# Optimization experiments

Hardware: AMD Instinct MI355X
Metric: run time of the kernel (lower is better)

The kernel has to match this reference:

```python
import jax, jax.numpy as jnp
import numpy as np

DET = 512       # detector bins
N_THETA = 180   # projection angles, theta = 0..179 degrees (1 deg spacing)


def _ramp_filter(size):
    """skimage _get_fourier_filter(size, 'ramp'): spatial ramp -> FFT."""
    n = np.concatenate((np.arange(1, size // 2 + 1, 2),
                        np.arange(size // 2 - 1, 0, -2)))
    f = np.zeros(size)
    f[0] = 0.25
    f[1::2] = -1.0 / (np.pi * n) ** 2
    return jnp.asarray(2.0 * np.real(np.fft.fft(f)), dtype=jnp.float32)


def _iradon(x):
    B, C, det, A = x.shape
    theta = jnp.deg2rad(jnp.arange(A, dtype=jnp.float32))  # 0..179 deg

    # --- ramp filtering along the detector axis ---
    size = max(64, int(2 ** np.ceil(np.log2(2 * det))))  # 1024 for det=512
    filt = _ramp_filter(size)                            # (size,)
    xp = jnp.pad(x, ((0, 0), (0, 0), (0, size - det), (0, 0)))
    proj_f = jnp.fft.fft(xp, axis=2) * filt[None, None, :, None]
    filtered = jnp.real(jnp.fft.ifft(proj_f, axis=2))[:, :, :det, :]  # (B,C,det,A)

    # --- backprojection (circle=False) ---
    out_size = int(np.floor(np.sqrt(det ** 2 / 2.0)))  # 362
    radius = out_size // 2
    xpr = jnp.arange(out_size, dtype=jnp.float32)[:, None] - radius  # rows
    ypr = jnp.arange(out_size, dtype=jnp.float32)[None, :] - radius  # cols
    cos_t = jnp.cos(theta)
    sin_t = jnp.sin(theta)
    # detector coordinate for every (angle, pixel): t = y*cos - x*sin
    t = ypr[None] * cos_t[:, None, None] - xpr[None] * sin_t[:, None, None]  # (A,out,out)
    pos = t + det // 2          # index into detector axis (x = arange(det)-det//2)
    i0 = jnp.floor(pos).astype(jnp.int32)
    frac = pos - i0.astype(jnp.float32)
    in_range = ((pos >= 0) & (pos <= det - 1)).astype(jnp.float32)  # fill_value=0 outside
    i0c = jnp.clip(i0, 0, det - 1)
    i1c = jnp.clip(i0 + 1, 0, det - 1)

    P = out_size * out_size
    ft = jnp.moveaxis(filtered, 3, 2)                     # (B,C,A,det)
    idx0 = jnp.broadcast_to(i0c.reshape(A, P)[None, None], (B, C, A, P))
    idx1 = jnp.broadcast_to(i1c.reshape(A, P)[None, None], (B, C, A, P))
    g0 = jnp.take_along_axis(ft, idx0, axis=3)            # (B,C,A,P)
    g1 = jnp.take_along_axis(ft, idx1, axis=3)
    w = frac.reshape(A, P)[None, None]
    m = in_range.reshape(A, P)[None, None]
    val = ((1.0 - w) * g0 + w * g1) * m                   # bilinear-in-1D interp, 0 outside
    recon = val.sum(axis=2).reshape(B, C, out_size, out_size)
    return recon * (jnp.pi / (2.0 * A))


def setup_inputs() -> dict:
    key = jax.random.key(0)
    x = jax.random.normal(key, (4, 1, DET, N_THETA), dtype=jnp.float32)
    return {"x": x}


def reference(x):
    return _iradon(x)
```

## Files before the change

kernel.cpp:

```cpp
#include <hip/hip_runtime.h>
#include <math.h>

#define DET 512
#define NA  180
#define OUT 362
#define RAD 181

#define NSPLIT 3
#define APB    60
#define CHUNK  10
#define LSTRIDE 516

constexpr double PI_D = 3.14159265358979323846;

constexpr double tsin(double x) {
    double x2 = x * x;
    return x * (1.0 + x2 * (-1.0/6 + x2 * (1.0/120 + x2 * (-1.0/5040 +
               x2 * (1.0/362880 + x2 * (-1.0/39916800))))));
}
constexpr double tcos(double x) {
    double x2 = x * x;
    return 1.0 + x2 * (-0.5 + x2 * (1.0/24 + x2 * (-1.0/720 +
               x2 * (1.0/40320 + x2 * (-1.0/3628800)))));
}

struct alignas(16) Trig { float c[NA]; float s[NA]; };
constexpr Trig make_trig() {
    Trig t{};
    constexpr double r = PI_D / 180.0;
    for (int k = 0; k < NA; ++k) {
        double c, s;
        if (k <= 45)       { c =  tcos(k * r);          s =  tsin(k * r); }
        else if (k <= 90)  { c =  tsin((90 - k) * r);   s =  tcos((90 - k) * r); }
        else if (k <= 135) { c = -tsin((k - 90) * r);   s =  tcos((k - 90) * r); }
        else               { c = -tcos((180 - k) * r);  s =  tsin((180 - k) * r); }
        t.c[k] = (float)c; t.s[k] = (float)s;
    }
    return t;
}
__device__ constexpr Trig TRIG = make_trig();

struct alignas(16) WTab { float w[2 * 127 * 8]; };
constexpr WTab make_wtab() {
    WTab t{};
    for (int h = 0; h < 2; ++h)
        for (int ui = 0; ui < 127; ++ui)
            for (int di = 0; di < 8; ++di) {
                int m = 8 * (ui - 63) + 2 * (di - 3) - 1 + 2 * h;
                double md = (double)m;
                t.w[(h * 127 + ui) * 8 + di] =
                    (float)(-2.0 / (PI_D * PI_D * md * md));
            }
    return t;
}
__device__ constexpr WTab WTAB = make_wtab();

__global__ __launch_bounds__(128) void ramp_filter_kernel(
        const float* __restrict__ x, float* __restrict__ ft,
        float* __restrict__ out, int n4, int pb4) {
    const int bx = blockIdx.x;
    const int b  = blockIdx.y;
    const int t  = threadIdx.x;

    const int rr = bx & 7, qq = bx >> 3;
    const int a  = 22 * rr + min(rr, 4) + qq;

    {
        float4* oz = (float4*)out;
        const float4 z4 = make_float4(0.f, 0.f, 0.f, 0.f);
        const int base4 = (b * NA + bx) * pb4;
        for (int i = t; i < pb4; i += 128) {
            int idx = base4 + i;
            if (idx < n4) oz[idx] = z4;
        }
    }

    __shared__ float Ef[768];
    __shared__ float Of[768];

    const float2 z2 = make_float2(0.f, 0.f);
    *(float2*)&Ef[2 * t]       = z2;
    *(float2*)&Ef[512 + 2 * t] = z2;
    *(float2*)&Of[2 * t]       = z2;
    *(float2*)&Of[512 + 2 * t] = z2;

    const float* xc = x + (size_t)(b * DET) * NA + a;
    float v0 = xc[(4 * t + 0) * NA];
    float v1 = xc[(4 * t + 1) * NA];
    float v2 = xc[(4 * t + 2) * NA];
    float v3 = xc[(4 * t + 3) * NA];
    *(float2*)&Ef[256 + 2 * t] = make_float2(v0, v2);
    *(float2*)&Of[256 + 2 * t] = make_float2(v1, v3);
    __syncthreads();

    const int half = __builtin_amdgcn_readfirstlane(t >> 6);
    const int tp   = t & 63;
    const float4* src4  = (const float4*)(half ? Ef : Of);
    const float4* self4 = (const float4*)(half ? Of : Ef);
    const float* __restrict__ Wh = WTAB.w + half * (127 * 8);

    float acc0 = 0.f, acc1 = 0.f, acc2 = 0.f, acc3 = 0.f;
    #pragma unroll 2
    for (int ui = 0; ui < 127; ++ui) {
        const float4 w0 = *(const float4*)&Wh[ui * 8];
        const float4 w1 = *(const float4*)&Wh[ui * 8 + 4];
        float4 s4 = src4[tp + (127 - ui)];
        acc0 = fmaf(s4.x, w0.w, fmaf(s4.y, w0.z, fmaf(s4.z, w0.y, fmaf(s4.w, w0.x, acc0))));
        acc1 = fmaf(s4.x, w1.x, fmaf(s4.y, w0.w, fmaf(s4.z, w0.z, fmaf(s4.w, w0.y, acc1))));
        acc2 = fmaf(s4.x, w1.y, fmaf(s4.y, w1.x, fmaf(s4.z, w0.w, fmaf(s4.w, w0.z, acc2))));
        acc3 = fmaf(s4.x, w1.z, fmaf(s4.y, w1.y, fmaf(s4.z, w1.x, fmaf(s4.w, w0.w, acc3))));
    }

    float4 sf = self4[64 + tp];
    acc0 = fmaf(0.5f, sf.x, acc0);
    acc1 = fmaf(0.5f, sf.y, acc1);
    acc2 = fmaf(0.5f, sf.z, acc2);
    acc3 = fmaf(0.5f, sf.w, acc3);

    float* o = ft + (b * NA + a) * DET + 8 * tp + half;
    o[0] = acc0;
    o[2] = acc1;
    o[4] = acc2;
    o[6] = acc3;
}

__device__ __forceinline__ float interp_fast(const float* __restrict__ L, float pos) {
    float fr = __builtin_amdgcn_fractf(pos);
    int   i0 = (int)pos;
    float g0 = L[i0];
    float g1 = L[i0 + 1];
    return fmaf(fr, g1 - g0, g0);
}
__device__ __forceinline__ float interp_masked(const float* __restrict__ L, float pos) {
    float v = interp_fast(L, pos);
    return pos <= (float)(DET - 1) ? v : 0.0f;
}

__global__ __launch_bounds__(256) void backproject_kernel(
        const float* __restrict__ ft, float* __restrict__ out) {
    const int bz = blockIdx.z;
    const int b  = bz / NSPLIT;
    const int sp = bz - b * NSPLIT;
    const int r0 = blockIdx.y * 32;
    const int c0 = blockIdx.x * 32;
    const int tid = threadIdx.x;
    const int tx = tid & 15;
    const int ty = tid >> 4;

    __shared__ float line[CHUNK][LSTRIDE];

    if (tid < CHUNK) line[tid][512] = 0.0f;

    const float xpr = (float)(min(r0 + ty, OUT - 1) - RAD);
    const float ypr = (float)(min(c0 + tx, OUT - 1) - RAD);

    float a00 = 0.0f, a01 = 0.0f, a10 = 0.0f, a11 = 0.0f;

    const float* base = ft + (b * NA + sp * APB) * DET;

    auto run = [&](auto&& interp) {
        for (int rd = 0; rd < APB / CHUNK; ++rd) {
            __syncthreads();
            const float* gsrc = base + rd * CHUNK * DET;
            #pragma unroll
            for (int k = 0; k < 5; ++k) {
                int j4 = tid + k * 256;
                float4 v = *(const float4*)&gsrc[j4 * 4];
                int ci = j4 >> 7;
                int d  = (j4 & 127) << 2;
                *(float4*)&line[ci][d] = v;
            }
            __syncthreads();

            const int abase = sp * APB + rd * CHUNK;
            #pragma unroll
            for (int i = 0; i < CHUNK; ++i) {
                const float cv = TRIG.c[abase + i];
                const float sv = TRIG.s[abase + i];
                float p00 = fmaf(ypr, cv, fmaf(xpr, -sv, 256.0f));
                float p01 = fmaf(16.0f, cv, p00);
                float p10 = fmaf(-16.0f, sv, p00);
                float p11 = fmaf(-16.0f, sv, p01);
                const float* L = line[i];
                a00 += interp(L, p00);
                a01 += interp(L, p01);
                a10 += interp(L, p10);
                a11 += interp(L, p11);
            }
        }
    };

    {
        float drm = fmaxf(fabsf((float)(r0 - RAD)),
                          fabsf((float)(min(r0 + 31, OUT - 1) - RAD)));
        float dcm = fmaxf(fabsf((float)(c0 - RAD)),
                          fabsf((float)(min(c0 + 31, OUT - 1) - RAD)));
        if (drm * drm + dcm * dcm <= 65025.0f)
            run([](const float* __restrict__ L, float p) { return interp_fast(L, p); });
        else
            run([](const float* __restrict__ L, float p) { return interp_masked(L, p); });
    }

    const float scale = (float)(PI_D / (2.0 * NA));
    const int r = r0 + ty;
    const int c = c0 + tx;
    float* ob = out + b * OUT * OUT;
    if (r < OUT) {
        if (c < OUT)      atomicAdd(&ob[r * OUT + c],      a00 * scale);
        if (c + 16 < OUT) atomicAdd(&ob[r * OUT + c + 16], a01 * scale);
    }
    if (r + 16 < OUT) {
        if (c < OUT)      atomicAdd(&ob[(r + 16) * OUT + c],      a10 * scale);
        if (c + 16 < OUT) atomicAdd(&ob[(r + 16) * OUT + c + 16], a11 * scale);
    }
}

extern "C" void kernel_launch(void* const* d_in, const int* in_sizes, int n_in,
                              void* d_out, int out_size, void* d_ws, size_t ws_size,
                              hipStream_t stream) {
    const float* x = (const float*)d_in[0];
    float* ft  = (float*)d_ws;
    float* out = (float*)d_out;

    const int B = in_sizes[0] / (DET * NA);

    const int n4  = out_size / 4;
    const int pb4 = (n4 + NA * B - 1) / (NA * B);

    ramp_filter_kernel<<<dim3(NA, B), 128, 0, stream>>>(x, ft, out, n4, pb4);
    backproject_kernel<<<dim3((OUT + 31) / 32, (OUT + 31) / 32, B * NSPLIT),
                         256, 0, stream>>>(ft, out);
}
```

Before: 109.8 us.

## Store filtered sinogram as neighbor pairs and gather directly from global memory

The filter kernel now writes each detector sample together with its right neighbour as a float2 (padded row stride), so backprojection can fetch both interpolation taps with one 8-byte load. Backprojection drops its LDS staging and block barriers and reads the paired rows straight from global/L2 memory. The filter kernel also doubles its threads and splits the convolution loop across two waves, combining partial sums through shared memory. The trade-off is that gathers now depend on cache hit rates rather than LDS, and the workspace is twice as large.

Result: slower. 121.1 us (+10.3%).

```diff
diff --git a/kernel.cpp b/kernel.cpp
--- a/kernel.cpp
+++ b/kernel.cpp
@@ -8,8 +8,7 @@
 
 #define NSPLIT 3
 #define APB    60
-#define CHUNK  10
-#define LSTRIDE 516
+#define FTP_LD 516
 
 constexpr double PI_D = 3.14159265358979323846;
 
@@ -55,8 +54,8 @@
 }
 __device__ constexpr WTab WTAB = make_wtab();
 
-__global__ __launch_bounds__(128) void ramp_filter_kernel(
-        const float* __restrict__ x, float* __restrict__ ft,
+__global__ __launch_bounds__(256) void ramp_filter_kernel(
+        const float* __restrict__ x, float2* __restrict__ ftp,
         float* __restrict__ out, int n4, int pb4) {
     const int bx = blockIdx.x;
     const int b  = blockIdx.y;
@@ -69,7 +68,7 @@
         float4* oz = (float4*)out;
         const float4 z4 = make_float4(0.f, 0.f, 0.f, 0.f);
         const int base4 = (b * NA + bx) * pb4;
-        for (int i = t; i < pb4; i += 128) {
+        for (int i = t; i < pb4; i += 256) {
             int idx = base4 + i;
             if (idx < n4) oz[idx] = z4;
         }
@@ -77,31 +76,30 @@
 
     __shared__ float Ef[768];
     __shared__ float Of[768];
-
-    const float2 z2 = make_float2(0.f, 0.f);
-    *(float2*)&Ef[2 * t]       = z2;
-    *(float2*)&Ef[512 + 2 * t] = z2;
-    *(float2*)&Of[2 * t]       = z2;
-    *(float2*)&Of[512 + 2 * t] = z2;
+    __shared__ float4 Rbuf[2][64];
+
+    Ef[t] = 0.f;  Ef[512 + t] = 0.f;
+    Of[t] = 0.f;  Of[512 + t] = 0.f;
 
     const float* xc = x + (size_t)(b * DET) * NA + a;
-    float v0 = xc[(4 * t + 0) * NA];
-    float v1 = xc[(4 * t + 1) * NA];
-    float v2 = xc[(4 * t + 2) * NA];
-    float v3 = xc[(4 * t + 3) * NA];
-    *(float2*)&Ef[256 + 2 * t] = make_float2(v0, v2);
-    *(float2*)&Of[256 + 2 * t] = make_float2(v1, v3);
+    float ev = xc[(2 * t) * NA];
+    float ov = xc[(2 * t + 1) * NA];
+    Ef[256 + t] = ev;
+    Of[256 + t] = ov;
     __syncthreads();
 
-    const int half = __builtin_amdgcn_readfirstlane(t >> 6);
+    const int half = __builtin_amdgcn_readfirstlane(t >> 7);
+    const int wseg = __builtin_amdgcn_readfirstlane((t >> 6) & 1);
     const int tp   = t & 63;
     const float4* src4  = (const float4*)(half ? Ef : Of);
     const float4* self4 = (const float4*)(half ? Of : Ef);
     const float* __restrict__ Wh = WTAB.w + half * (127 * 8);
 
     float acc0 = 0.f, acc1 = 0.f, acc2 = 0.f, acc3 = 0.f;
+    const int uiBeg = wseg ? 64 : 0;
+    const int uiEnd = wseg ? 127 : 64;
     #pragma unroll 2
-    for (int ui = 0; ui < 127; ++ui) {
+    for (int ui = uiBeg; ui < uiEnd; ++ui) {
         const float4 w0 = *(const float4*)&Wh[ui * 8];
         const float4 w1 = *(const float4*)&Wh[ui * 8 + 4];
         float4 s4 = src4[tp + (127 - ui)];
@@ -111,33 +109,44 @@
         acc3 = fmaf(s4.x, w1.z, fmaf(s4.y, w1.y, fmaf(s4.z, w1.x, fmaf(s4.w, w0.w, acc3))));
     }
 
-    float4 sf = self4[64 + tp];
-    acc0 = fmaf(0.5f, sf.x, acc0);
-    acc1 = fmaf(0.5f, sf.y, acc1);
-    acc2 = fmaf(0.5f, sf.z, acc2);
-    acc3 = fmaf(0.5f, sf.w, acc3);
-
-    float* o = ft + (b * NA + a) * DET + 8 * tp + half;
-    o[0] = acc0;
-    o[2] = acc1;
-    o[4] = acc2;
-    o[6] = acc3;
-}
-
-__device__ __forceinline__ float interp_fast(const float* __restrict__ L, float pos) {
+    if (wseg) {
+        Rbuf[half][tp] = make_float4(acc0, acc1, acc2, acc3);
+    } else {
+        float4 sf = self4[64 + tp];
+        acc0 = fmaf(0.5f, sf.x, acc0);
+        acc1 = fmaf(0.5f, sf.y, acc1);
+        acc2 = fmaf(0.5f, sf.z, acc2);
+        acc3 = fmaf(0.5f, sf.w, acc3);
+    }
+    __syncthreads();
+
+    if (!wseg) {
+        float4 r = Rbuf[half][tp];
+        acc0 += r.x; acc1 += r.y; acc2 += r.z; acc3 += r.w;
+
+        float2* fp = ftp + (size_t)(b * NA + a) * FTP_LD;
+        const int d0 = 8 * tp + half;
+        fp[d0].x = acc0;  if (d0 > 0) fp[d0 - 1].y = acc0;
+        fp[d0 + 2].x = acc1;  fp[d0 + 1].y = acc1;
+        fp[d0 + 4].x = acc2;  fp[d0 + 3].y = acc2;
+        fp[d0 + 6].x = acc3;  fp[d0 + 5].y = acc3;
+        if (d0 + 6 == 511) fp[511].y = 0.0f;
+    }
+}
+
+__device__ __forceinline__ float interp_fast(const float2* __restrict__ L, float pos) {
     float fr = __builtin_amdgcn_fractf(pos);
     int   i0 = (int)pos;
-    float g0 = L[i0];
-    float g1 = L[i0 + 1];
-    return fmaf(fr, g1 - g0, g0);
-}
-__device__ __forceinline__ float interp_masked(const float* __restrict__ L, float pos) {
+    float2 g = L[i0];
+    return fmaf(fr, g.y - g.x, g.x);
+}
+__device__ __forceinline__ float interp_masked(const float2* __restrict__ L, float pos) {
     float v = interp_fast(L, pos);
     return pos <= (float)(DET - 1) ? v : 0.0f;
 }
 
 __global__ __launch_bounds__(256) void backproject_kernel(
-        const float* __restrict__ ft, float* __restrict__ out) {
+        const float2* __restrict__ ftp, float* __restrict__ out) {
     const int bz = blockIdx.z;
     const int b  = bz / NSPLIT;
     const int sp = bz - b * NSPLIT;
@@ -147,46 +156,28 @@
     const int tx = tid & 15;
     const int ty = tid >> 4;
 
-    __shared__ float line[CHUNK][LSTRIDE];
-
-    if (tid < CHUNK) line[tid][512] = 0.0f;
-
     const float xpr = (float)(min(r0 + ty, OUT - 1) - RAD);
     const float ypr = (float)(min(c0 + tx, OUT - 1) - RAD);
 
     float a00 = 0.0f, a01 = 0.0f, a10 = 0.0f, a11 = 0.0f;
 
-    const float* base = ft + (b * NA + sp * APB) * DET;
+    const float2* baseP = ftp + (size_t)(b * NA + sp * APB) * FTP_LD;
+    const int abase = sp * APB;
 
     auto run = [&](auto&& interp) {
-        for (int rd = 0; rd < APB / CHUNK; ++rd) {
-            __syncthreads();
-            const float* gsrc = base + rd * CHUNK * DET;
-            #pragma unroll
-            for (int k = 0; k < 5; ++k) {
-                int j4 = tid + k * 256;
-                float4 v = *(const float4*)&gsrc[j4 * 4];
-                int ci = j4 >> 7;
-                int d  = (j4 & 127) << 2;
-                *(float4*)&line[ci][d] = v;
-            }
-            __syncthreads();
-
-            const int abase = sp * APB + rd * CHUNK;
-            #pragma unroll
-            for (int i = 0; i < CHUNK; ++i) {
-                const float cv = TRIG.c[abase + i];
-                const float sv = TRIG.s[abase + i];
-                float p00 = fmaf(ypr, cv, fmaf(xpr, -sv, 256.0f));
-                float p01 = fmaf(16.0f, cv, p00);
-                float p10 = fmaf(-16.0f, sv, p00);
-                float p11 = fmaf(-16.0f, sv, p01);
-                const float* L = line[i];
-                a00 += interp(L, p00);
-                a01 += interp(L, p01);
-                a10 += interp(L, p10);
-                a11 += interp(L, p11);
-            }
+        #pragma unroll 4
+        for (int i = 0; i < APB; ++i) {
+            const float cv = TRIG.c[abase + i];
+            const float sv = TRIG.s[abase + i];
+            const float2* Lp = baseP + (size_t)i * FTP_LD;
+            float p00 = fmaf(ypr, cv, fmaf(xpr, -sv, 256.0f));
+            float p01 = fmaf(16.0f, cv, p00);
+            float p10 = fmaf(-16.0f, sv, p00);
+            float p11 = fmaf(-16.0f, sv, p01);
+            a00 += interp(Lp, p00);
+            a01 += interp(Lp, p01);
+            a10 += interp(Lp, p10);
+            a11 += interp(Lp, p11);
         }
     };
 
@@ -196,9 +187,9 @@
         float dcm = fmaxf(fabsf((float)(c0 - RAD)),
                           fabsf((float)(min(c0 + 31, OUT - 1) - RAD)));
         if (drm * drm + dcm * dcm <= 65025.0f)
-            run([](const float* __restrict__ L, float p) { return interp_fast(L, p); });
+            run([](const float2* __restrict__ L, float p) { return interp_fast(L, p); });
         else
-            run([](const float* __restrict__ L, float p) { return interp_masked(L, p); });
+            run([](const float2* __restrict__ L, float p) { return interp_masked(L, p); });
     }
 
     const float scale = (float)(PI_D / (2.0 * NA));
@@ -219,15 +210,15 @@
                               void* d_out, int out_size, void* d_ws, size_t ws_size,
                               hipStream_t stream) {
     const float* x = (const float*)d_in[0];
-    float* ft  = (float*)d_ws;
-    float* out = (float*)d_out;
+    float2* ftp = (float2*)d_ws;
+    float* out  = (float*)d_out;
 
     const int B = in_sizes[0] / (DET * NA);
 
     const int n4  = out_size / 4;
     const int pb4 = (n4 + NA * B - 1) / (NA * B);
 
-    ramp_filter_kernel<<<dim3(NA, B), 128, 0, stream>>>(x, ft, out, n4, pb4);
+    ramp_filter_kernel<<<dim3(NA, B), 256, 0, stream>>>(x, ftp, out, n4, pb4);
     backproject_kernel<<<dim3((OUT + 31) / 32, (OUT + 31) / 32, B * NSPLIT),
-                         256, 0, stream>>>(ft, out);
-}
+                         256, 0, stream>>>(ftp, out);
+}
```
